# Optimization experiments

Hardware: AMD Instinct MI355X
Metric: run time of the kernel (lower is better)

The kernel has to match this reference:

```python
import jax, jax.numpy as jnp
import numpy as np

B, S, L, C, H, D, CP = 32, 4, 64, 32, 4, 8, 16  # batch, tracks, bins, c_msa, heads, d_head, c_pair


def _ln(x, g, b, eps=1e-5):
    m = jnp.mean(x, axis=-1, keepdims=True)
    v = jnp.mean((x - m) ** 2, axis=-1, keepdims=True)
    return (x - m) / jnp.sqrt(v + eps) * g + b


def setup_inputs() -> dict:
    key = jax.random.key(0)
    ks = jax.random.split(key, 20)
    n = lambda k, shape, s=0.1: jax.random.normal(k, shape, jnp.float32) * s
    return dict(
        chip_ctcf=n(ks[0], (B, L), 1.0),
        chip_hac=n(ks[1], (B, L), 1.0),
        chip_me1=n(ks[2], (B, L), 1.0),
        chip_me3=n(ks[3], (B, L), 1.0),
        bulk_map=n(ks[4], (B, 1, L, L), 1.0),
        we_w=n(ks[5], (C, 1)), we_b=jnp.zeros((C,), jnp.float32),
        pos=n(ks[6], (1, 1, L, C)),
        mn_g=jnp.ones((C,), jnp.float32), mn_b=jnp.zeros((C,), jnp.float32),
        wq=n(ks[7], (C, C)), bq=jnp.zeros((C,), jnp.float32),
        wk=n(ks[8], (C, C)), bk=jnp.zeros((C,), jnp.float32),
        wv=n(ks[9], (C, C)), bv=jnp.zeros((C,), jnp.float32),
        wo=n(ks[10], (C, C)), bo=jnp.zeros((C,), jnp.float32),
        an_g=jnp.ones((C,), jnp.float32), an_b=jnp.zeros((C,), jnp.float32),
        conv_w=n(ks[11], (H,)), conv_b=jnp.zeros((H,), jnp.float32),
        gate_w=n(ks[12], (H, D, D)), gate_b=jnp.zeros((H, D), jnp.float32),
        pp_w=n(ks[13], (CP, C * C), 0.03), pp_b=jnp.zeros((CP,), jnp.float32),
        ada_g=jnp.ones((CP,), jnp.float32), ada_b=jnp.zeros((CP,), jnp.float32),
        ada_alpha=jnp.ones((1,), jnp.float32),
    )


def reference(chip_ctcf, chip_hac, chip_me1, chip_me3, bulk_map,
              we_w, we_b, pos, mn_g, mn_b,
              wq, bq, wk, bk, wv, bv, wo, bo, an_g, an_b,
              conv_w, conv_b, gate_w, gate_b,
              pp_w, pp_b, ada_g, ada_b, ada_alpha):
    # 1) build MSA: (B, S=4, L, C)
    signals = jnp.stack([chip_ctcf, chip_hac, chip_me1, chip_me3], axis=1)  # (B,S,L)
    msa = signals[..., None] * we_w[:, 0] + we_b                            # Linear(1,C)
    x = _ln(msa + pos, mn_g, mn_b)                                          # (B,S,L,C)

    # 2) row self-attention with bulk-derived per-head bias
    q = (x @ wq.T + bq).reshape(B, S, L, H, D)
    k = (x @ wk.T + bk).reshape(B, S, L, H, D)
    v = (x @ wv.T + bv).reshape(B, S, L, H, D)
    scores = jnp.einsum('bslhd,bsmhd->bshlm', q, k) / jnp.sqrt(jnp.float32(D))
    bias = bulk_map * conv_w.reshape(1, H, 1, 1) + conv_b.reshape(1, H, 1, 1)  # 1x1 conv -> (B,H,L,L)
    attn = jax.nn.softmax(scores + bias[:, None], axis=-1)                     # (B,S,H,L,L)
    out = jnp.einsum('bshlm,bsmhd->bshld', attn, v)
    gate = jax.nn.sigmoid(jnp.einsum('hcd,bshld->bshlc', gate_w, out)
                          + gate_b[None, None, :, None, :])
    out = out * gate
    out = out.transpose(0, 1, 3, 2, 4).reshape(B, S, L, C)
    out = out @ wo.T + bo
    x = _ln(x + out, an_g, an_b)                                            # post-attn LayerNorm

    # 3) outer-product (of max over tracks) pair features
    m = jnp.max(x, axis=1)                                                  # (B,L,C)
    pair = jnp.einsum('bic,bjd->bijcd', m, m).reshape(B, L, L, C * C)       # (B,L,L,1024)
    nrm = jnp.sqrt(jnp.sum(pair * pair, axis=-1, keepdims=True))
    pair = pair / jnp.maximum(nrm, 1e-6)                                    # F.normalize
    feat = pair @ pp_w.T + pp_b                                             # (B,L,L,CP)
    feat = feat + ada_alpha * _ln(feat, ada_g, ada_b)                       # AdaNorm
    feat = jax.nn.silu(feat)
    return feat.transpose(0, 3, 1, 2)                                       # (B,CP,L,L)
```

## Files before the change

### kernel.cpp

```cpp
#include <hip/hip_runtime.h>
#include <hip/hip_bf16.h>

#define NB 32
#define NS 4
#define NL 64
#define NC 32
#define NH 4
#define ND 8
#define NCP 16

using fp = const float* __restrict__;

__global__ __launch_bounds__(512) void k1_attn(
    fp ctcf, fp hac, fp me1, fp me3, fp bulk,
    fp we_w, fp we_b, fp pos, fp mn_g, fp mn_b,
    fp wq, fp bq, fp wk, fp bk, fp wv, fp bv,
    fp wo, fp bo, fp an_g, fp an_b,
    fp conv_w, fp conv_b, fp gate_w, fp gate_b,
    float* __restrict__ xpostT)
{
    __shared__ float qs_s[NC*NL];
    __shared__ float ks_s[NC*NL];
    __shared__ float vs_s[NC*NL];
    __shared__ float xs_s[NC*NL];
    __shared__ float ao_s[NC*NL];
    __shared__ float bulk_s[32*65];
    __shared__ float red1[32*17], red2[32*17];
    __shared__ float mstat[32], istat[32];

    const int t    = threadIdx.x;
    const int w    = t >> 6;
    const int l    = t & 63;
    const int bx   = blockIdx.x;
    const int b    = bx >> 3;
    const int s    = (bx >> 1) & 3;
    const int half = bx & 1;

    for (int idx = t; idx < 32*NL; idx += 512){
        int lr = idx >> 6, m = idx & 63;
        bulk_s[lr*65 + m] = bulk[b*NL*NL + (half*32 + lr)*NL + m];
    }

    fp sigp = (s == 0) ? ctcf : (s == 1) ? hac : (s == 2) ? me1 : me3;
    const float sig = sigp[b*NL + l];

    float x[NC];
    float mean = 0.f;
#pragma unroll
    for (int c = 0; c < NC; c++){
        x[c] = sig * we_w[c] + we_b[c] + pos[l*NC + c];
        mean += x[c];
    }
    mean *= (1.f/NC);
    float var = 0.f;
#pragma unroll
    for (int c = 0; c < NC; c++){ float d = x[c] - mean; var += d*d; }
    var *= (1.f/NC);
    float inv = rsqrtf(var + 1e-5f);
#pragma unroll
    for (int c = 0; c < NC; c++) x[c] = (x[c] - mean)*inv*mn_g[c] + mn_b[c];

#pragma unroll
    for (int c = 0; c < NC; c++)
        if ((c >> 2) == w) xs_s[c*NL + l] = x[c];

#pragma unroll
    for (int e4 = 0; e4 < 4; e4++){
        int e = w*4 + e4;
        float aq = bq[e], ak = bk[e], av = bv[e];
#pragma unroll
        for (int c = 0; c < NC; c++){
            float xv = x[c];
            aq += xv * wq[e*NC + c];
            ak += xv * wk[e*NC + c];
            av += xv * wv[e*NC + c];
        }
        qs_s[e*NL + l] = aq;
        ks_s[e*NL + l] = ak;
        vs_s[e*NL + l] = av;
    }
    __syncthreads();

    const int h   = w >> 1;
    const int sub = ((w & 1) << 6) | l;
    const int rl  = sub >> 2;
    const int q4  = sub & 3;
    const int r   = half*32 + rl;
    const int m0  = q4*16;

    float q8[ND];
#pragma unroll
    for (int d = 0; d < ND; d++) q8[d] = qs_s[(h*ND + d)*NL + r];

    const float rs8 = 0.35355339059327373f;
    const float cw = conv_w[h], cb = conv_b[h];
    float srow[16];
    float mx = -1e30f;
#pragma unroll
    for (int mi = 0; mi < 16; mi++){
        int m = m0 + mi;
        float dot = 0.f;
#pragma unroll
        for (int d = 0; d < ND; d++)
            dot += q8[d] * ks_s[(h*ND + d)*NL + m];
        float v = dot*rs8 + bulk_s[rl*65 + m]*cw + cb;
        srow[mi] = v;
        mx = fmaxf(mx, v);
    }
    mx = fmaxf(mx, __shfl_xor(mx, 1));
    mx = fmaxf(mx, __shfl_xor(mx, 2));
    float sm = 0.f;
#pragma unroll
    for (int mi = 0; mi < 16; mi++){ srow[mi] = __expf(srow[mi] - mx); sm += srow[mi]; }
    sm += __shfl_xor(sm, 1);
    sm += __shfl_xor(sm, 2);
    float is = 1.f / sm;

    float o[ND];
#pragma unroll
    for (int d = 0; d < ND; d++) o[d] = 0.f;
#pragma unroll
    for (int mi = 0; mi < 16; mi++){
        float a = srow[mi] * is;
#pragma unroll
        for (int d = 0; d < ND; d++)
            o[d] += a * vs_s[(h*ND + d)*NL + m0 + mi];
    }
#pragma unroll
    for (int d = 0; d < ND; d++){
        o[d] += __shfl_xor(o[d], 1);
        o[d] += __shfl_xor(o[d], 2);
    }

#pragma unroll
    for (int c8 = 0; c8 < ND; c8++){
        float g = gate_b[h*ND + c8];
#pragma unroll
        for (int d = 0; d < ND; d++) g += gate_w[(h*ND + c8)*ND + d] * o[d];
        float val = o[c8] * (1.f/(1.f + __expf(-g)));
        if ((c8 >> 1) == q4) ao_s[(h*ND + c8)*NL + r] = val;
    }
    __syncthreads();

    const int r3  = t & 31;
    const int rg  = half*32 + r3;
    const int cg  = t >> 5;
    float vals[2];
    float psum = 0.f, psq = 0.f;
#pragma unroll
    for (int k = 0; k < 2; k++){
        int c = cg*2 + k;
        float a = bo[c];
#pragma unroll
        for (int e = 0; e < NC; e++) a += ao_s[e*NL + rg] * wo[c*NC + e];
        float val = xs_s[c*NL + rg] + a;
        vals[k] = val; psum += val; psq += val*val;
    }
    red1[r3*17 + cg] = psum;
    red2[r3*17 + cg] = psq;
    __syncthreads();
    if (t < 32){
        float sum = 0.f, ssq = 0.f;
#pragma unroll
        for (int g = 0; g < 16; g++){ sum += red1[t*17 + g]; ssq += red2[t*17 + g]; }
        float mn = sum * (1.f/NC);
        float vr = ssq * (1.f/NC) - mn*mn;
        mstat[t] = mn;
        istat[t] = rsqrtf(vr + 1e-5f);
    }
    __syncthreads();
    {
        float mn = mstat[r3], iv = istat[r3];
#pragma unroll
        for (int k = 0; k < 2; k++){
            int c = cg*2 + k;
            xpostT[((b*NS + s)*NC + c)*NL + rg] = (vals[k] - mn)*iv*an_g[c] + an_b[c];
        }
    }
}

__global__ __launch_bounds__(256) void k23_pair(
    const float* __restrict__ xpostT, fp pp_w,
    fp pp_b, fp ada_g, fp ada_b, fp ada_alpha,
    float* __restrict__ out)
{
    __shared__ float ppws[8*NC*NC];
    __shared__ float mh[NC*NL];
    __shared__ float u[NCP*4*NC];

    const int b  = blockIdx.x >> 4;
    const int it = blockIdx.x & 15;
    const int t  = threadIdx.x;
    const int w  = t >> 6;
    const int j  = t & 63;

    const float* xb = xpostT + b*NS*NC*NL;
#pragma unroll
    for (int k = 0; k < 8; k++){
        int cj = k*256 + t;
        float v = xb[cj];
        v = fmaxf(v, xb[NC*NL + cj]);
        v = fmaxf(v, xb[2*NC*NL + cj]);
        v = fmaxf(v, xb[3*NC*NL + cj]);
        mh[cj] = v;
    }
    __syncthreads();

    if (t < NL){
        float sq = 0.f;
#pragma unroll
        for (int c = 0; c < NC; c++){ float v = mh[c*NL + t]; sq += v*v; }
        u[t] = 1.f / fmaxf(sqrtf(sq), 1e-3f);
    }
    {
        const float4* src = (const float4*)(pp_w);
        float4* dst = (float4*)ppws;
#pragma unroll
        for (int k = 0; k < 8; k++) dst[k*256 + t] = src[k*256 + t];
    }
    __syncthreads();

#pragma unroll
    for (int k = 0; k < 8; k++){
        int cj = k*256 + t;
        mh[cj] *= u[cj & 63];
    }
    __syncthreads();

    float md[NC];
#pragma unroll
    for (int c = 0; c < NC; c++) md[c] = mh[c*NL + j];

#pragma unroll
    for (int loop = 0; loop < 4; loop++){
        int idx = loop*256 + t;
        int d  = idx & 31;
        int ip = (idx >> 5) & 3;
        int pl = idx >> 7;
        int i  = it*4 + ip;
        float acc = 0.f;
#pragma unroll
        for (int c = 0; c < NC; c++)
            acc += mh[c*NL + i] * ppws[pl*1024 + c*32 + d];
        u[pl*128 + ip*32 + d] = acc;
    }
    __syncthreads();

    {
        const float4* src = (const float4*)(pp_w + 8*NC*NC);
        float4* dst = (float4*)ppws;
#pragma unroll
        for (int k = 0; k < 8; k++) dst[k*256 + t] = src[k*256 + t];
    }
    __syncthreads();

#pragma unroll
    for (int loop = 0; loop < 4; loop++){
        int idx = loop*256 + t;
        int d  = idx & 31;
        int ip = (idx >> 5) & 3;
        int pl = idx >> 7;
        int i  = it*4 + ip;
        float acc = 0.f;
#pragma unroll
        for (int c = 0; c < NC; c++)
            acc += mh[c*NL + i] * ppws[pl*1024 + c*32 + d];
        u[(8 + pl)*128 + ip*32 + d] = acc;
    }
    __syncthreads();

    float f[NCP];
#pragma unroll 1
    for (int p = 0; p < NCP; p++){
        float a = 0.f;
#pragma unroll
        for (int d = 0; d < NC; d++)
            a += u[p*128 + w*32 + d] * md[d];
        f[p] = a;
    }

    const float alpha = ada_alpha[0];
    float fsum = 0.f, fsq = 0.f;
#pragma unroll
    for (int p = 0; p < NCP; p++){
        float v = f[p] + pp_b[p];
        f[p] = v; fsum += v; fsq += v*v;
    }
    float fmean = fsum * (1.f/NCP);
    float fvar  = fsq * (1.f/NCP) - fmean*fmean;
    float finv  = rsqrtf(fvar + 1e-5f);
    const int i = it*4 + w;
#pragma unroll
    for (int p = 0; p < NCP; p++){
        float v = f[p] + alpha * ((f[p] - fmean)*finv*ada_g[p] + ada_b[p]);
        out[((b*NCP + p)*NL + i)*NL + j] = v / (1.f + __expf(-v));
    }
}

extern "C" void kernel_launch(void* const* d_in, const int* in_sizes, int n_in,
                              void* d_out, int out_size, void* d_ws, size_t ws_size,
                              hipStream_t stream)
{
    float* xpostT = (float*)d_ws;

    k1_attn<<<NB*NS*2, 512, 0, stream>>>(
        (fp)d_in[0], (fp)d_in[1], (fp)d_in[2], (fp)d_in[3], (fp)d_in[4],
        (fp)d_in[5], (fp)d_in[6], (fp)d_in[7], (fp)d_in[8], (fp)d_in[9],
        (fp)d_in[10], (fp)d_in[11], (fp)d_in[12], (fp)d_in[13], (fp)d_in[14], (fp)d_in[15],
        (fp)d_in[16], (fp)d_in[17], (fp)d_in[18], (fp)d_in[19],
        (fp)d_in[20], (fp)d_in[21], (fp)d_in[22], (fp)d_in[23], xpostT);

    k23_pair<<<NB*16, 256, 0, stream>>>(
        xpostT, (fp)d_in[24], (fp)d_in[25], (fp)d_in[26], (fp)d_in[27], (fp)d_in[28],
        (float*)d_out);
}
```

Before: 143.1 us.

## Restructure attention and pair kernels with row-major swizzled LDS and vector loads

The attention kernel now stores q/k/v/x and gated output row-major with padded, XOR-swizzled shared-memory layouts and float4 accesses. The output projection and LayerNorm reduction use shuffles instead of shared-memory reductions, and the intermediate is written as (row, channel). The pair kernel reads this new layout with float4 loads and prefetches both weight halves into registers to overlap global loads. It also drops the explicit normalization pass, instead scaling by 1/max(|m_i||m_j|, eps) at the end. This raises register pressure, and the norm clamp semantics now differ slightly from the previous per-vector clamp.

```diff
diff --git a/kernel.cpp b/kernel.cpp
--- a/kernel.cpp
+++ b/kernel.cpp
@@ -19,14 +19,12 @@
     fp conv_w, fp conv_b, fp gate_w, fp gate_b,
     float* __restrict__ xpostT)
 {
-    __shared__ float qs_s[NC*NL];
-    __shared__ float ks_s[NC*NL];
-    __shared__ float vs_s[NC*NL];
-    __shared__ float xs_s[NC*NL];
-    __shared__ float ao_s[NC*NL];
-    __shared__ float bulk_s[32*65];
-    __shared__ float red1[32*17], red2[32*17];
-    __shared__ float mstat[32], istat[32];
+    __shared__ float q2[NL*36];
+    __shared__ float k2[NL*36];
+    __shared__ float v2[NL*36];
+    __shared__ float x2[NL*36];
+    __shared__ float a2[NL*36];
+    __shared__ float bs[32*NL];
 
     const int t    = threadIdx.x;
     const int w    = t >> 6;
@@ -36,10 +34,7 @@
     const int s    = (bx >> 1) & 3;
     const int half = bx & 1;
 
-    for (int idx = t; idx < 32*NL; idx += 512){
-        int lr = idx >> 6, m = idx & 63;
-        bulk_s[lr*65 + m] = bulk[b*NL*NL + (half*32 + lr)*NL + m];
-    }
+    ((float4*)bs)[t] = ((const float4*)(bulk + b*NL*NL + half*32*NL))[t];
 
     fp sigp = (s == 0) ? ctcf : (s == 1) ? hac : (s == 2) ? me1 : me3;
     const float sig = sigp[b*NL + l];
@@ -47,9 +42,15 @@
     float x[NC];
     float mean = 0.f;
 #pragma unroll
-    for (int c = 0; c < NC; c++){
-        x[c] = sig * we_w[c] + we_b[c] + pos[l*NC + c];
-        mean += x[c];
+    for (int k4 = 0; k4 < 8; k4++){
+        float4 ww = ((const float4*)we_w)[k4];
+        float4 wb = ((const float4*)we_b)[k4];
+        float4 pp = ((const float4*)pos)[l*8 + k4];
+        x[4*k4+0] = sig*ww.x + wb.x + pp.x;
+        x[4*k4+1] = sig*ww.y + wb.y + pp.y;
+        x[4*k4+2] = sig*ww.z + wb.z + pp.z;
+        x[4*k4+3] = sig*ww.w + wb.w + pp.w;
+        mean += x[4*k4+0] + x[4*k4+1] + x[4*k4+2] + x[4*k4+3];
     }
     mean *= (1.f/NC);
     float var = 0.f;
@@ -58,124 +59,153 @@
     var *= (1.f/NC);
     float inv = rsqrtf(var + 1e-5f);
 #pragma unroll
-    for (int c = 0; c < NC; c++) x[c] = (x[c] - mean)*inv*mn_g[c] + mn_b[c];
-
-#pragma unroll
-    for (int c = 0; c < NC; c++)
-        if ((c >> 2) == w) xs_s[c*NL + l] = x[c];
-
+    for (int k4 = 0; k4 < 8; k4++){
+        float4 gg = ((const float4*)mn_g)[k4];
+        float4 bb = ((const float4*)mn_b)[k4];
+        x[4*k4+0] = (x[4*k4+0] - mean)*inv*gg.x + bb.x;
+        x[4*k4+1] = (x[4*k4+1] - mean)*inv*gg.y + bb.y;
+        x[4*k4+2] = (x[4*k4+2] - mean)*inv*gg.z + bb.z;
+        x[4*k4+3] = (x[4*k4+3] - mean)*inv*gg.w + bb.w;
+    }
+
+    float aqv[4], akv[4], avv[4];
 #pragma unroll
     for (int e4 = 0; e4 < 4; e4++){
-        int e = w*4 + e4;
+        const int e = (w << 2) + e4;
         float aq = bq[e], ak = bk[e], av = bv[e];
 #pragma unroll
-        for (int c = 0; c < NC; c++){
-            float xv = x[c];
-            aq += xv * wq[e*NC + c];
-            ak += xv * wk[e*NC + c];
-            av += xv * wv[e*NC + c];
-        }
-        qs_s[e*NL + l] = aq;
-        ks_s[e*NL + l] = ak;
-        vs_s[e*NL + l] = av;
-    }
-    __syncthreads();
-
-    const int h   = w >> 1;
-    const int sub = ((w & 1) << 6) | l;
-    const int rl  = sub >> 2;
-    const int q4  = sub & 3;
-    const int r   = half*32 + rl;
-    const int m0  = q4*16;
-
-    float q8[ND];
-#pragma unroll
-    for (int d = 0; d < ND; d++) q8[d] = qs_s[(h*ND + d)*NL + r];
-
-    const float rs8 = 0.35355339059327373f;
-    const float cw = conv_w[h], cb = conv_b[h];
-    float srow[16];
-    float mx = -1e30f;
-#pragma unroll
-    for (int mi = 0; mi < 16; mi++){
-        int m = m0 + mi;
-        float dot = 0.f;
-#pragma unroll
-        for (int d = 0; d < ND; d++)
-            dot += q8[d] * ks_s[(h*ND + d)*NL + m];
-        float v = dot*rs8 + bulk_s[rl*65 + m]*cw + cb;
-        srow[mi] = v;
-        mx = fmaxf(mx, v);
-    }
-    mx = fmaxf(mx, __shfl_xor(mx, 1));
-    mx = fmaxf(mx, __shfl_xor(mx, 2));
-    float sm = 0.f;
-#pragma unroll
-    for (int mi = 0; mi < 16; mi++){ srow[mi] = __expf(srow[mi] - mx); sm += srow[mi]; }
-    sm += __shfl_xor(sm, 1);
-    sm += __shfl_xor(sm, 2);
-    float is = 1.f / sm;
-
-    float o[ND];
-#pragma unroll
-    for (int d = 0; d < ND; d++) o[d] = 0.f;
-#pragma unroll
-    for (int mi = 0; mi < 16; mi++){
-        float a = srow[mi] * is;
-#pragma unroll
-        for (int d = 0; d < ND; d++)
-            o[d] += a * vs_s[(h*ND + d)*NL + m0 + mi];
-    }
-#pragma unroll
-    for (int d = 0; d < ND; d++){
-        o[d] += __shfl_xor(o[d], 1);
-        o[d] += __shfl_xor(o[d], 2);
-    }
-
-#pragma unroll
-    for (int c8 = 0; c8 < ND; c8++){
-        float g = gate_b[h*ND + c8];
-#pragma unroll
-        for (int d = 0; d < ND; d++) g += gate_w[(h*ND + c8)*ND + d] * o[d];
-        float val = o[c8] * (1.f/(1.f + __expf(-g)));
-        if ((c8 >> 1) == q4) ao_s[(h*ND + c8)*NL + r] = val;
-    }
-    __syncthreads();
-
-    const int r3  = t & 31;
-    const int rg  = half*32 + r3;
-    const int cg  = t >> 5;
-    float vals[2];
-    float psum = 0.f, psq = 0.f;
-#pragma unroll
-    for (int k = 0; k < 2; k++){
-        int c = cg*2 + k;
-        float a = bo[c];
-#pragma unroll
-        for (int e = 0; e < NC; e++) a += ao_s[e*NL + rg] * wo[c*NC + e];
-        float val = xs_s[c*NL + rg] + a;
-        vals[k] = val; psum += val; psq += val*val;
-    }
-    red1[r3*17 + cg] = psum;
-    red2[r3*17 + cg] = psq;
-    __syncthreads();
-    if (t < 32){
-        float sum = 0.f, ssq = 0.f;
-#pragma unroll
-        for (int g = 0; g < 16; g++){ sum += red1[t*17 + g]; ssq += red2[t*17 + g]; }
-        float mn = sum * (1.f/NC);
-        float vr = ssq * (1.f/NC) - mn*mn;
-        mstat[t] = mn;
-        istat[t] = rsqrtf(vr + 1e-5f);
-    }
-    __syncthreads();
+        for (int k4 = 0; k4 < 8; k4++){
+            float4 wq4 = ((const float4*)(wq + e*NC))[k4];
+            float4 wk4 = ((const float4*)(wk + e*NC))[k4];
+            float4 wv4 = ((const float4*)(wv + e*NC))[k4];
+            float x0 = x[4*k4+0], x1 = x[4*k4+1], x2v = x[4*k4+2], x3 = x[4*k4+3];
+            aq += wq4.x*x0 + wq4.y*x1 + wq4.z*x2v + wq4.w*x3;
+            ak += wk4.x*x0 + wk4.y*x1 + wk4.z*x2v + wk4.w*x3;
+            av += wv4.x*x0 + wv4.y*x1 + wv4.z*x2v + wv4.w*x3;
+        }
+        aqv[e4] = aq; akv[e4] = ak; avv[e4] = av;
+    }
     {
-        float mn = mstat[r3], iv = istat[r3];
-#pragma unroll
-        for (int k = 0; k < 2; k++){
-            int c = cg*2 + k;
-            xpostT[((b*NS + s)*NC + c)*NL + rg] = (vals[k] - mn)*iv*an_g[c] + an_b[c];
-        }
+        const int slt = ((w >> 1) ^ (l >> 4));
+        const int kh  = (w & 1);
+        const int off = l*36 + slt*8 + kh*4;
+        *(float4*)&q2[off] = make_float4(aqv[0], aqv[1], aqv[2], aqv[3]);
+        *(float4*)&k2[off] = make_float4(akv[0], akv[1], akv[2], akv[3]);
+        *(float4*)&v2[off] = make_float4(avv[0], avv[1], avv[2], avv[3]);
+        float xa = 0.f, xb2 = 0.f, xc = 0.f, xd = 0.f;
+#pragma unroll
+        for (int ww = 0; ww < 8; ww++)
+            if (ww == w){ xa = x[4*ww]; xb2 = x[4*ww+1]; xc = x[4*ww+2]; xd = x[4*ww+3]; }
+        *(float4*)&x2[l*36 + ((w ^ (l >> 4)) << 2)] = make_float4(xa, xb2, xc, xd);
+    }
+    __syncthreads();
+
+    {
+        const int h   = w >> 1;
+        const int sub = ((w & 1) << 6) | l;
+        const int rl  = sub >> 2;
+        const int q4  = sub & 3;
+        const int r   = half*32 + rl;
+        const int m0  = q4 << 4;
+
+        const int qoff = r*36 + ((h ^ (r >> 4)) << 3);
+        float4 qa = *(const float4*)&q2[qoff];
+        float4 qb = *(const float4*)&q2[qoff + 4];
+
+        const float rs8 = 0.35355339059327373f;
+        const float cw = conv_w[h], cb = conv_b[h];
+        float srow[16];
+        float mx = -1e30f;
+#pragma unroll
+        for (int mi = 0; mi < 16; mi++){
+            int m  = m0 + mi;
+            int kb = m*36 + ((h ^ (m >> 4)) << 3);
+            float4 ka  = *(const float4*)&k2[kb];
+            float4 kb4 = *(const float4*)&k2[kb + 4];
+            float dot = qa.x*ka.x + qa.y*ka.y + qa.z*ka.z + qa.w*ka.w
+                      + qb.x*kb4.x + qb.y*kb4.y + qb.z*kb4.z + qb.w*kb4.w;
+            float vv = dot*rs8 + bs[rl*64 + m]*cw + cb;
+            srow[mi] = vv;
+            mx = fmaxf(mx, vv);
+        }
+        mx = fmaxf(mx, __shfl_xor(mx, 1));
+        mx = fmaxf(mx, __shfl_xor(mx, 2));
+        float sm = 0.f;
+#pragma unroll
+        for (int mi = 0; mi < 16; mi++){ srow[mi] = __expf(srow[mi] - mx); sm += srow[mi]; }
+        sm += __shfl_xor(sm, 1);
+        sm += __shfl_xor(sm, 2);
+        float is = 1.f / sm;
+
+        float4 oa = make_float4(0.f,0.f,0.f,0.f);
+        float4 ob = make_float4(0.f,0.f,0.f,0.f);
+#pragma unroll
+        for (int mi = 0; mi < 16; mi++){
+            int m  = m0 + mi;
+            int vb = m*36 + ((h ^ (m >> 4)) << 3);
+            float a = srow[mi] * is;
+            float4 va  = *(const float4*)&v2[vb];
+            float4 vb4 = *(const float4*)&v2[vb + 4];
+            oa.x += a*va.x;  oa.y += a*va.y;  oa.z += a*va.z;  oa.w += a*va.w;
+            ob.x += a*vb4.x; ob.y += a*vb4.y; ob.z += a*vb4.z; ob.w += a*vb4.w;
+        }
+#define RED2(f) f += __shfl_xor(f, 1); f += __shfl_xor(f, 2);
+        RED2(oa.x) RED2(oa.y) RED2(oa.z) RED2(oa.w)
+        RED2(ob.x) RED2(ob.y) RED2(ob.z) RED2(ob.w)
+#undef RED2
+
+        const int c8l = q4 << 1;
+        const float* gwl = gate_w + (h*ND + c8l)*ND;
+        float4 g1 = *(const float4*)gwl;
+        float4 g2 = *(const float4*)(gwl + 4);
+        float4 g3 = *(const float4*)(gwl + 8);
+        float4 g4 = *(const float4*)(gwl + 12);
+        float gl = gate_b[h*ND + c8l]
+                 + g1.x*oa.x + g1.y*oa.y + g1.z*oa.z + g1.w*oa.w
+                 + g2.x*ob.x + g2.y*ob.y + g2.z*ob.z + g2.w*ob.w;
+        float gh = gate_b[h*ND + c8l + 1]
+                 + g3.x*oa.x + g3.y*oa.y + g3.z*oa.z + g3.w*oa.w
+                 + g4.x*ob.x + g4.y*ob.y + g4.z*ob.z + g4.w*ob.w;
+        float olo, ohi;
+        if      (q4 == 0){ olo = oa.x; ohi = oa.y; }
+        else if (q4 == 1){ olo = oa.z; ohi = oa.w; }
+        else if (q4 == 2){ olo = ob.x; ohi = ob.y; }
+        else             { olo = ob.z; ohi = ob.w; }
+        float vlo = olo * (1.f/(1.f + __expf(-gl)));
+        float vhi = ohi * (1.f/(1.f + __expf(-gh)));
+        *(float2*)&a2[r*36 + h*8 + c8l] = make_float2(vlo, vhi);
+    }
+    __syncthreads();
+
+    {
+        const int rg = t >> 4;
+        const int cg = t & 15;
+        const int r3 = half*32 + rg;
+        const int c0 = cg << 1;
+        float accL = bo[c0], accH = bo[c0+1];
+#pragma unroll
+        for (int k4 = 0; k4 < 8; k4++){
+            float4 av = *(const float4*)&a2[r3*36 + (k4 << 2)];
+            float4 w1 = ((const float4*)(wo + c0*NC))[k4];
+            float4 w2 = ((const float4*)(wo + (c0+1)*NC))[k4];
+            accL += av.x*w1.x + av.y*w1.y + av.z*w1.z + av.w*w1.w;
+            accH += av.x*w2.x + av.y*w2.y + av.z*w2.z + av.w*w2.w;
+        }
+        float2 xr = *(const float2*)&x2[r3*36 + (((cg >> 1) ^ (r3 >> 4)) << 2) + ((cg & 1) << 1)];
+        float vlo = xr.x + accL;
+        float vhi = xr.y + accH;
+        float ps = vlo + vhi, pq = vlo*vlo + vhi*vhi;
+        ps += __shfl_xor(ps, 1);  pq += __shfl_xor(pq, 1);
+        ps += __shfl_xor(ps, 2);  pq += __shfl_xor(pq, 2);
+        ps += __shfl_xor(ps, 4);  pq += __shfl_xor(pq, 4);
+        ps += __shfl_xor(ps, 8);  pq += __shfl_xor(pq, 8);
+        float mn = ps * (1.f/NC);
+        float vr = pq * (1.f/NC) - mn*mn;
+        float iv = rsqrtf(vr + 1e-5f);
+        float2 og;
+        og.x = (vlo - mn)*iv*an_g[c0]   + an_b[c0];
+        og.y = (vhi - mn)*iv*an_g[c0+1] + an_b[c0+1];
+        *(float2*)&xpostT[((b*NS + s)*NL + r3)*NC + c0] = og;
     }
 }
 
@@ -185,8 +215,9 @@
     float* __restrict__ out)
 {
     __shared__ float ppws[8*NC*NC];
-    __shared__ float mh[NC*NL];
+    __shared__ float mh[NC*66];
     __shared__ float u[NCP*4*NC];
+    __shared__ float nrm_s[NL];
 
     const int b  = blockIdx.x >> 4;
     const int it = blockIdx.x & 15;
@@ -194,42 +225,42 @@
     const int w  = t >> 6;
     const int j  = t & 63;
 
-    const float* xb = xpostT + b*NS*NC*NL;
-#pragma unroll
-    for (int k = 0; k < 8; k++){
-        int cj = k*256 + t;
-        float v = xb[cj];
-        v = fmaxf(v, xb[NC*NL + cj]);
-        v = fmaxf(v, xb[2*NC*NL + cj]);
-        v = fmaxf(v, xb[3*NC*NL + cj]);
-        mh[cj] = v;
-    }
+    float4 s1[8];
+#pragma unroll
+    for (int k = 0; k < 8; k++) s1[k] = ((const float4*)pp_w)[k*256 + t];
+
+    const float4* xb4 = (const float4*)(xpostT + b*NS*NL*NC);
+#pragma unroll
+    for (int k = 0; k < 2; k++){
+        int idx = k*256 + t;
+        float4 v0 = xb4[idx];
+        float4 v1 = xb4[512  + idx];
+        float4 v2 = xb4[1024 + idx];
+        float4 v3 = xb4[1536 + idx];
+        float m0 = fmaxf(fmaxf(v0.x, v1.x), fmaxf(v2.x, v3.x));
+        float m1 = fmaxf(fmaxf(v0.y, v1.y), fmaxf(v2.y, v3.y));
+        float m2 = fmaxf(fmaxf(v0.z, v1.z), fmaxf(v2.z, v3.z));
+        float m3 = fmaxf(fmaxf(v0.w, v1.w), fmaxf(v2.w, v3.w));
+        int l = idx >> 3, c4 = idx & 7;
+        mh[(4*c4+0)*66 + l] = m0;
+        mh[(4*c4+1)*66 + l] = m1;
+        mh[(4*c4+2)*66 + l] = m2;
+        mh[(4*c4+3)*66 + l] = m3;
+    }
+#pragma unroll
+    for (int k = 0; k < 8; k++) ((float4*)ppws)[k*256 + t] = s1[k];
     __syncthreads();
 
     if (t < NL){
         float sq = 0.f;
 #pragma unroll
-        for (int c = 0; c < NC; c++){ float v = mh[c*NL + t]; sq += v*v; }
-        u[t] = 1.f / fmaxf(sqrtf(sq), 1e-3f);
-    }
-    {
-        const float4* src = (const float4*)(pp_w);
-        float4* dst = (float4*)ppws;
-#pragma unroll
-        for (int k = 0; k < 8; k++) dst[k*256 + t] = src[k*256 + t];
-    }
-    __syncthreads();
-
-#pragma unroll
-    for (int k = 0; k < 8; k++){
-        int cj = k*256 + t;
-        mh[cj] *= u[cj & 63];
-    }
-    __syncthreads();
-
-    float md[NC];
-#pragma unroll
-    for (int c = 0; c < NC; c++) md[c] = mh[c*NL + j];
+        for (int c = 0; c < NC; c++){ float v = mh[c*66 + t]; sq += v*v; }
+        nrm_s[t] = sqrtf(sq);
+    }
+
+    float4 s2[8];
+#pragma unroll
+    for (int k = 0; k < 8; k++) s2[k] = ((const float4*)pp_w)[2048 + k*256 + t];
 
 #pragma unroll
     for (int loop = 0; loop < 4; loop++){
@@ -241,17 +272,12 @@
         float acc = 0.f;
 #pragma unroll
         for (int c = 0; c < NC; c++)
-            acc += mh[c*NL + i] * ppws[pl*1024 + c*32 + d];
+            acc += mh[c*66 + i] * ppws[pl*1024 + c*32 + d];
         u[pl*128 + ip*32 + d] = acc;
     }
     __syncthreads();
-
-    {
-        const float4* src = (const float4*)(pp_w + 8*NC*NC);
-        float4* dst = (float4*)ppws;
-#pragma unroll
-        for (int k = 0; k < 8; k++) dst[k*256 + t] = src[k*256 + t];
-    }
+#pragma unroll
+    for (int k = 0; k < 8; k++) ((float4*)ppws)[k*256 + t] = s2[k];
     __syncthreads();
 
 #pragma unroll
@@ -264,32 +290,39 @@
         float acc = 0.f;
 #pragma unroll
         for (int c = 0; c < NC; c++)
-            acc += mh[c*NL + i] * ppws[pl*1024 + c*32 + d];
+            acc += mh[c*66 + i] * ppws[pl*1024 + c*32 + d];
         u[(8 + pl)*128 + ip*32 + d] = acc;
     }
     __syncthreads();
 
+    float md[NC];
+#pragma unroll
+    for (int c = 0; c < NC; c++) md[c] = mh[c*66 + j];
+
+    const int i = it*4 + w;
     float f[NCP];
-#pragma unroll 1
+#pragma unroll
     for (int p = 0; p < NCP; p++){
         float a = 0.f;
 #pragma unroll
-        for (int d = 0; d < NC; d++)
-            a += u[p*128 + w*32 + d] * md[d];
+        for (int k4 = 0; k4 < 8; k4++){
+            float4 uv = *(const float4*)&u[p*128 + w*32 + (k4 << 2)];
+            a += uv.x*md[4*k4+0] + uv.y*md[4*k4+1] + uv.z*md[4*k4+2] + uv.w*md[4*k4+3];
+        }
         f[p] = a;
     }
 
+    const float sc = 1.f / fmaxf(nrm_s[i] * nrm_s[j], 1e-6f);
     const float alpha = ada_alpha[0];
     float fsum = 0.f, fsq = 0.f;
 #pragma unroll
     for (int p = 0; p < NCP; p++){
-        float v = f[p] + pp_b[p];
+        float v = f[p]*sc + pp_b[p];
         f[p] = v; fsum += v; fsq += v*v;
     }
     float fmean = fsum * (1.f/NCP);
     float fvar  = fsq * (1.f/NCP) - fmean*fmean;
     float finv  = rsqrtf(fvar + 1e-5f);
-    const int i = it*4 + w;
 #pragma unroll
     for (int p = 0; p < NCP; p++){
         float v = f[p] + alpha * ((f[p] - fmean)*finv*ada_g[p] + ada_b[p]);
```

Result: slower. 147.3 us (+3.0%).
